# Kernel tuning notes

Measured on AMD Instinct MI355X. Metric: run time of the kernel, lower is better.

## Reference

```python
import jax, jax.numpy as jnp
import numpy as np

N = 100000      # nodes
E = 800000      # directed edges (avg in-degree 8)
FIN = 2         # node features: [type, requests]
C = 32          # embedding_size (per-head out channels)
H = 4           # heads
HC = H * C      # 128
L = 3           # extra conv layers after conv1
D1, D2 = 128, 64
NL = 15         # num_locations
BN_EPS = 1e-5


def _tconv(x, src, dst, ea, qw, qb, kw, kb, vw, vb, ew, skw, skb, bw):
    """PyG TransformerConv with heads=H, concat=True, beta=True, edge_dim."""
    n = x.shape[0]
    q = (x @ qw.T + qb).reshape(n, H, C)
    k = (x @ kw.T + kb).reshape(n, H, C)
    v = (x @ vw.T + vb).reshape(n, H, C)
    e = (ea @ ew.T).reshape(-1, H, C)                     # [E,H,C], lin_edge has no bias
    ke = k[src] + e
    alpha = (q[dst] * ke).sum(-1) / jnp.sqrt(jnp.float32(C))   # [E,H]
    # scatter-softmax over incoming edges of each destination node
    amax = jax.ops.segment_max(alpha, dst, num_segments=n)     # [N,H]
    ex = jnp.exp(alpha - amax[dst])
    denom = jax.ops.segment_sum(ex, dst, num_segments=n)
    attn = ex / jnp.where(denom > 0, denom, 1.0)[dst]
    msg = (v[src] + e) * attn[..., None]                       # [E,H,C]
    out = jax.ops.segment_sum(msg, dst, num_segments=n).reshape(n, HC)
    skip = x @ skw.T + skb                                     # root transform
    beta = jax.nn.sigmoid(jnp.concatenate([out, skip, out - skip], -1) @ bw.T)  # [N,1]
    return beta * skip + (1.0 - beta) * out


def _bn(x, g, b):
    # BatchNorm1d with batch statistics (biased variance), as in torch training math
    mu = x.mean(0)
    var = ((x - mu) ** 2).mean(0)
    return (x - mu) / jnp.sqrt(var + BN_EPS) * g + b


def _forward(node_type, requests, latency, active_mask, edge_index, P):
    (q1_w, q1_b, k1_w, k1_b, v1_w, v1_b, e1_w, skip1_w, skip1_b, beta1_w,
     transf1_w, transf1_b, bn1_g, bn1_b,
     qL_w, qL_b, kL_w, kL_b, vL_w, vL_b, eL_w, skipL_w, skipL_b, betaL_w,
     transfL_w, transfL_b, bnL_g, bnL_b,
     lin1_w, lin1_b, lin2_w, lin2_b, rem_w, rem_b, addp_w, addp_b) = P
    src, dst = edge_index[0], edge_index[1]
    ea = latency[:, None]                                  # [E,1]
    x = jnp.stack([node_type, requests], 1)                # [N,2]
    x = _tconv(x, src, dst, ea, q1_w, q1_b, k1_w, k1_b, v1_w, v1_b,
               e1_w, skip1_w, skip1_b, beta1_w)
    x = _bn(jax.nn.relu(x @ transf1_w.T + transf1_b), bn1_g, bn1_b)
    for i in range(L):
        x = _tconv(x, src, dst, ea, qL_w[i], qL_b[i], kL_w[i], kL_b[i], vL_w[i], vL_b[i],
                   eL_w[i], skipL_w[i], skipL_b[i], betaL_w[i])
        x = _bn(jax.nn.relu(x @ transfL_w[i].T + transfL_b[i]), bnL_g[i], bnL_b[i])
    x = jax.nn.relu(x @ lin1_w.T + lin1_b)                 # dropout(p=0.8) is eval no-op
    x = jax.nn.relu(x @ lin2_w.T + lin2_b)                 # [N,D2]
    mask = active_mask
    head = mask[:NL]
    rm_head = jnp.where(head == 0.0, -jnp.inf, jnp.where(jnp.isneginf(head), 0.0, head))
    remove_mask = mask.at[:NL].set(rm_head)
    removed_logits = (x @ rem_w.T + rem_b)[:, 0] + remove_mask   # [N]
    k1, k2 = jax.random.split(jax.random.key(42))
    action1 = jax.random.categorical(k1, removed_logits)
    mask2 = mask.at[action1].set(0.0)
    proj = jnp.tanh(x[action1] @ addp_w.T + addp_b)              # [D2]
    new_logits = x @ proj + mask2                                # [N]
    action2 = jax.random.categorical(k2, new_logits)
    return removed_logits, new_logits, action1, action2


def setup_inputs() -> dict:
    key = jax.random.key(0)
    ks = iter(jax.random.split(key, 80))
    def nrm(shape, s=0.1):
        return jax.random.normal(next(ks), shape, jnp.float32) * s
    inp = {
        "node_type": jax.random.uniform(next(ks), (N,), jnp.float32),
        "requests": jax.random.uniform(next(ks), (N,), jnp.float32),
        "latency": jax.random.uniform(next(ks), (E,), jnp.float32),
        "active_mask": jnp.zeros((N,), jnp.float32),
        "edge_index": jax.random.randint(next(ks), (2, E), 0, N, dtype=jnp.int32),
        "q1_w": nrm((HC, FIN)), "q1_b": jnp.zeros((HC,)),
        "k1_w": nrm((HC, FIN)), "k1_b": jnp.zeros((HC,)),
        "v1_w": nrm((HC, FIN)), "v1_b": jnp.zeros((HC,)),
        "e1_w": nrm((HC, 1)),
        "skip1_w": nrm((HC, FIN)), "skip1_b": jnp.zeros((HC,)),
        "beta1_w": nrm((1, 3 * HC)),
        "transf1_w": nrm((C, HC)), "transf1_b": jnp.zeros((C,)),
        "bn1_g": jnp.ones((C,)), "bn1_b": jnp.zeros((C,)),
        "qL_w": nrm((L, HC, C)), "qL_b": jnp.zeros((L, HC)),
        "kL_w": nrm((L, HC, C)), "kL_b": jnp.zeros((L, HC)),
        "vL_w": nrm((L, HC, C)), "vL_b": jnp.zeros((L, HC)),
        "eL_w": nrm((L, HC, 1)),
        "skipL_w": nrm((L, HC, C)), "skipL_b": jnp.zeros((L, HC)),
        "betaL_w": nrm((L, 1, 3 * HC)),
        "transfL_w": nrm((L, C, HC)), "transfL_b": jnp.zeros((L, C)),
        "bnL_g": jnp.ones((L, C)), "bnL_b": jnp.zeros((L, C)),
        "lin1_w": nrm((D1, C)), "lin1_b": jnp.zeros((D1,)),
        "lin2_w": nrm((D2, D1)), "lin2_b": jnp.zeros((D2,)),
        "rem_w": nrm((1, D2)), "rem_b": jnp.zeros((1,)),
        "addp_w": nrm((D2, D2)), "addp_b": jnp.zeros((D2,)),
    }
    return inp


def reference(node_type, requests, latency, active_mask, edge_index,
              q1_w, q1_b, k1_w, k1_b, v1_w, v1_b, e1_w, skip1_w, skip1_b, beta1_w,
              transf1_w, transf1_b, bn1_g, bn1_b,
              qL_w, qL_b, kL_w, kL_b, vL_w, vL_b, eL_w, skipL_w, skipL_b, betaL_w,
              transfL_w, transfL_b, bnL_g, bnL_b,
              lin1_w, lin1_b, lin2_w, lin2_b, rem_w, rem_b, addp_w, addp_b):
    P = (q1_w, q1_b, k1_w, k1_b, v1_w, v1_b, e1_w, skip1_w, skip1_b, beta1_w,
         transf1_w, transf1_b, bn1_g, bn1_b,
         qL_w, qL_b, kL_w, kL_b, vL_w, vL_b, eL_w, skipL_w, skipL_b, betaL_w,
         transfL_w, transfL_b, bnL_g, bnL_b,
         lin1_w, lin1_b, lin2_w, lin2_b, rem_w, rem_b, addp_w, addp_b)
    rl, nl, a1, a2 = _forward(node_type, requests, latency, active_mask, edge_index, P)
    log_probs = jnp.stack([jax.nn.log_softmax(rl)[a1], jax.nn.log_softmax(nl)[a2]])
    logits = jnp.stack([rl, nl])      # [2,N]
    actions = jnp.stack([a1, a2])     # [2]
    return logits, actions, log_probs
```

## Files before the change

kernel.cpp:

```cpp
#include <hip/hip_runtime.h>
#include <hip/hip_bf16.h>
#include <math.h>
#include <stdint.h>
#include <limits.h>

#define NN 100000
#define NE 800000
#define PB 512
#define NDB 512
#define NEGBIG (-1e30f)

typedef __hip_bfloat16 bf16;

__device__ __forceinline__ float bf2f(unsigned short u)
{
  union { unsigned v; float f; } x; x.v = ((unsigned)u) << 16; return x.f;
}
__device__ __forceinline__ unsigned short f2bf(float f)
{
  bf16 h = __float2bfloat16(f);
  return *reinterpret_cast<unsigned short*>(&h);
}
__device__ __forceinline__ unsigned pk2(float a, float b)
{
  return (unsigned)f2bf(a) | ((unsigned)f2bf(b) << 16);
}

__device__ __forceinline__ uint2 tf_dev(unsigned k0, unsigned k1, unsigned x0, unsigned x1)
{
  const unsigned ks2 = k0 ^ k1 ^ 0x1BD11BDAu;
#define TFR(r) { x0 += x1; x1 = (x1 << r) | (x1 >> (32 - r)); x1 ^= x0; }
  x0 += k0; x1 += k1;
  TFR(13) TFR(15) TFR(26) TFR(6)
  x0 += k1; x1 += ks2 + 1u;
  TFR(17) TFR(29) TFR(16) TFR(24)
  x0 += ks2; x1 += k0 + 2u;
  TFR(13) TFR(15) TFR(26) TFR(6)
  x0 += k0; x1 += k1 + 3u;
  TFR(17) TFR(29) TFR(16) TFR(24)
  x0 += k1; x1 += ks2 + 4u;
  TFR(13) TFR(15) TFR(26) TFR(6)
  x0 += ks2; x1 += k0 + 5u;
#undef TFR
  return make_uint2(x0, x1);
}

static void tf_host(unsigned k0, unsigned k1, unsigned x0, unsigned x1,
                    unsigned* o0, unsigned* o1)
{
  const unsigned ks2 = k0 ^ k1 ^ 0x1BD11BDAu;
#define TFR(r) { x0 += x1; x1 = (x1 << r) | (x1 >> (32 - r)); x1 ^= x0; }
  x0 += k0; x1 += k1;
  TFR(13) TFR(15) TFR(26) TFR(6)
  x0 += k1; x1 += ks2 + 1u;
  TFR(17) TFR(29) TFR(16) TFR(24)
  x0 += ks2; x1 += k0 + 2u;
  TFR(13) TFR(15) TFR(26) TFR(6)
  x0 += k0; x1 += k1 + 3u;
  TFR(17) TFR(29) TFR(16) TFR(24)
  x0 += k1; x1 += ks2 + 4u;
  TFR(13) TFR(15) TFR(26) TFR(6)
  x0 += ks2; x1 += k0 + 5u;
#undef TFR
  *o0 = x0; *o1 = x1;
}

__device__ __forceinline__ float gumbel_of(unsigned ka, unsigned kb, int i)
{
  uint2 c = tf_dev(ka, kb, 0u, (unsigned)i);
  unsigned bits = c.x ^ c.y;
  float f = __uint_as_float((bits >> 9) | 0x3f800000u) - 1.0f;
  const float TINYF = 1.17549435e-38f;
  float u = fmaxf(TINYF, f + TINYF);
  return -logf(-logf(u));
}

__global__ __launch_bounds__(256) void k_zero2(int* __restrict__ a, int* __restrict__ b)
{
  int i = blockIdx.x * 256 + threadIdx.x;
  if (i < NN) { a[i] = 0; b[i] = 0; }
}

__global__ __launch_bounds__(256) void k_hist(const int* __restrict__ edst, int* __restrict__ deg)
{
  int e = blockIdx.x * 256 + threadIdx.x;
  if (e < NE) atomicAdd(&deg[edst[e]], 1);
}

__global__ __launch_bounds__(1024) void k_scan(const int* __restrict__ deg, int* __restrict__ rowptr)
{
  __shared__ int wsum[16];
  __shared__ int chtot;
  const int t = threadIdx.x;
  const int lane = t & 63;
  const int wv = t >> 6;
  int carry = 0;
  for (int base = 0; base < NN; base += 4096) {
    int i0 = base + t * 4;
    int d0 = 0, d1 = 0, d2 = 0, d3 = 0;
    if (i0 + 3 < NN) { int4 dd = *(const int4*)(deg + i0); d0 = dd.x; d1 = dd.y; d2 = dd.z; d3 = dd.w; }
    else {
      if (i0     < NN) d0 = deg[i0];
      if (i0 + 1 < NN) d1 = deg[i0 + 1];
      if (i0 + 2 < NN) d2 = deg[i0 + 2];
      if (i0 + 3 < NN) d3 = deg[i0 + 3];
    }
    int tsum = d0 + d1 + d2 + d3;
    int sc = tsum;
    #pragma unroll
    for (int off = 1; off < 64; off <<= 1) { int o = __shfl_up(sc, off); if (lane >= off) sc += o; }
    if (lane == 63) wsum[wv] = sc;
    __syncthreads();
    if (wv == 0 && lane < 16) {
      int wval = wsum[lane];
      int wsc = wval;
      #pragma unroll
      for (int off = 1; off < 16; off <<= 1) { int o = __shfl_up(wsc, off); if (lane >= off) wsc += o; }
      if (lane == 15) chtot = wsc;
      wsum[lane] = wsc - wval;
    }
    __syncthreads();
    int excl = carry + wsum[wv] + (sc - tsum);
    if (i0     < NN) rowptr[i0]     = excl;
    if (i0 + 1 < NN) rowptr[i0 + 1] = excl + d0;
    if (i0 + 2 < NN) rowptr[i0 + 2] = excl + d0 + d1;
    if (i0 + 3 < NN) rowptr[i0 + 3] = excl + d0 + d1 + d2;
    carry += chtot;
    __syncthreads();
  }
  if (t == 0) rowptr[NN] = carry;
}

__global__ __launch_bounds__(256) void k_scatter(
    const int* __restrict__ esrc, const int* __restrict__ edst,
    const float* __restrict__ lat, const int* __restrict__ rowptr,
    int* __restrict__ fill, int2* __restrict__ csr)
{
  int e = blockIdx.x * 256 + threadIdx.x;
  if (e >= NE) return;
  int d = edst[e];
  int pos = rowptr[d] + atomicAdd(&fill[d], 1);
  csr[pos] = make_int2(esrc[e], __float_as_int(lat[e]));
}

__global__ __launch_bounds__(256) void k_qkvs_first(
    const float* __restrict__ nt, const float* __restrict__ rq,
    const float* __restrict__ qw, const float* __restrict__ qbv,
    const float* __restrict__ kw, const float* __restrict__ kbv,
    const float* __restrict__ vw, const float* __restrict__ vbv,
    const float* __restrict__ sw, const float* __restrict__ sbv,
    unsigned* __restrict__ q, unsigned short* __restrict__ kv, float* __restrict__ sk)
{
  int idx = blockIdx.x * 256 + threadIdx.x;
  if (idx >= NN * 64) return;
  int n = idx >> 6, l = idx & 63;
  int j0 = 2 * l, j1 = 2 * l + 1;
  float a = nt[n], b = rq[n];
  float q0 = (a * qw[2 * j0] + b * qw[2 * j0 + 1]) + qbv[j0];
  float q1 = (a * qw[2 * j1] + b * qw[2 * j1 + 1]) + qbv[j1];
  q[idx] = pk2(q0, q1);
  ushort4 kvo;
  kvo.x = f2bf((a * kw[2 * j0] + b * kw[2 * j0 + 1]) + kbv[j0]);
  kvo.y = f2bf((a * kw[2 * j1] + b * kw[2 * j1 + 1]) + kbv[j1]);
  kvo.z = f2bf((a * vw[2 * j0] + b * vw[2 * j0 + 1]) + vbv[j0]);
  kvo.w = f2bf((a * vw[2 * j1] + b * vw[2 * j1 + 1]) + vbv[j1]);
  ((ushort4*)kv)[idx] = kvo;
  float2 so;
  so.x = (a * sw[2 * j0] + b * sw[2 * j0 + 1]) + sbv[j0];
  so.y = (a * sw[2 * j1] + b * sw[2 * j1 + 1]) + sbv[j1];
  ((float2*)sk)[idx] = so;
}

#define QP 36
#define WP 33
__global__ __launch_bounds__(256) void k_qkvs3(
    const float* __restrict__ yb, const float* __restrict__ stats,
    const float* __restrict__ bng, const float* __restrict__ bnb,
    const float* __restrict__ wq, const float* __restrict__ bq,
    const float* __restrict__ wk, const float* __restrict__ bk,
    const float* __restrict__ wv, const float* __restrict__ bv,
    const float* __restrict__ wsk, const float* __restrict__ bsk,
    unsigned* __restrict__ oq, unsigned short* __restrict__ okv, float* __restrict__ os)
{
  __shared__ __align__(16) float xs[64 * QP];
  __shared__ __align__(16) float Wl[2 * 128 * WP];

  const int t = threadIdx.x;
  const int nq = t & 15;
  const int chq = t >> 4;
  const int y = blockIdx.y;

  if (y == 1) {
    for (int idx = t; idx < 128 * 32; idx += 256) {
      int c = idx >> 5, k = idx & 31;
      Wl[c * WP + k] = wk[idx];
      Wl[128 * WP + c * WP + k] = wv[idx];
    }
  } else {
    const float* W = (y == 0) ? wq : wsk;
    for (int idx = t; idx < 128 * 32; idx += 256) {
      int c = idx >> 5, k = idx & 31;
      Wl[c * WP + k] = W[idx];
    }
  }

  const int ch0 = (t & 7) * 4;
  float sc[4], sh[4];
  #pragma unroll
  for (int c = 0; c < 4; ++c) {
    int ch = ch0 + c;
    float rsig = 1.0f / stats[32 + ch];
    sc[c] = bng[ch] * rsig;
    sh[c] = bnb[ch] - stats[ch] * sc[c];
  }

  const int ntiles = (NN + 63) / 64;
  for (int tile = blockIdx.x; tile < ntiles; tile += gridDim.x) {
    const int base = tile * 64;
    __syncthreads();
    #pragma unroll
    for (int rep = 0; rep < 2; ++rep) {
      int f = t + rep * 256;
      int n = f >> 3, kq = f & 7;
      int gn = base + n;
      if (gn >= NN) gn = NN - 1;
      float4 v = *(const float4*)(yb + (size_t)gn * 32 + kq * 4);
      v.x = fmaf(v.x, sc[0], sh[0]);
      v.y = fmaf(v.y, sc[1], sh[1]);
      v.z = fmaf(v.z, sc[2], sh[2]);
      v.w = fmaf(v.w, sc[3], sh[3]);
      *(float4*)(xs + n * QP + kq * 4) = v;
    }
    __syncthreads();

    if (y == 1) {
      float ak[4][8], av[4][8];
      #pragma unroll
      for (int s = 0; s < 4; ++s)
        #pragma unroll
        for (int j = 0; j < 8; ++j) { ak[s][j] = bk[chq * 8 + j]; av[s][j] = bv[chq * 8 + j]; }
      #pragma unroll 4
      for (int k2 = 0; k2 < 16; ++k2) {
        const int k = 2 * k2;
        float2 xv[4];
        #pragma unroll
        for (int s = 0; s < 4; ++s) xv[s] = *(const float2*)(xs + (nq + 16 * s) * QP + k);
        #pragma unroll
        for (int j = 0; j < 8; ++j) {
          float2 wk2 = *(const float2*)(Wl + (chq * 8 + j) * WP + k);
          float2 wv2 = *(const float2*)(Wl + 128 * WP + (chq * 8 + j) * WP + k);
          #pragma unroll
          for (int s = 0; s < 4; ++s) {
            ak[s][j] = fmaf(xv[s].x, wk2.x, ak[s][j]);
            ak[s][j] = fmaf(xv[s].y, wk2.y, ak[s][j]);
            av[s][j] = fmaf(xv[s].x, wv2.x, av[s][j]);
            av[s][j] = fmaf(xv[s].y, wv2.y, av[s][j]);
          }
        }
      }
      #pragma unroll
      for (int s = 0; s < 4; ++s) {
        int node = base + nq + 16 * s;
        if (node < NN) {
          uint4 A, B;
          A.x = pk2(ak[s][0], ak[s][1]); A.y = pk2(av[s][0], av[s][1]);
          A.z = pk2(ak[s][2], ak[s][3]); A.w = pk2(av[s][2], av[s][3]);
          B.x = pk2(ak[s][4], ak[s][5]); B.y = pk2(av[s][4], av[s][5]);
          B.z = pk2(ak[s][6], ak[s][7]); B.w = pk2(av[s][6], av[s][7]);
          unsigned short* dst = okv + (size_t)node * 256 + chq * 16;
          *(uint4*)dst = A;
          *(uint4*)(dst + 8) = B;
        }
      }
    } else if (y == 0) {
      float acc[4][8];
      #pragma unroll
      for (int s = 0; s < 4; ++s)
        #pragma unroll
        for (int j = 0; j < 8; ++j) acc[s][j] = bq[chq * 8 + j];
      #pragma unroll 4
      for (int k2 = 0; k2 < 16; ++k2) {
        const int k = 2 * k2;
        float2 xv[4];
        #pragma unroll
        for (int s = 0; s < 4; ++s) xv[s] = *(const float2*)(xs + (nq + 16 * s) * QP + k);
        #pragma unroll
        for (int j = 0; j < 8; ++j) {
          float2 w2 = *(const float2*)(Wl + (chq * 8 + j) * WP + k);
          #pragma unroll
          for (int s = 0; s < 4; ++s) {
            acc[s][j] = fmaf(xv[s].x, w2.x, acc[s][j]);
            acc[s][j] = fmaf(xv[s].y, w2.y, acc[s][j]);
          }
        }
      }
      #pragma unroll
      for (int s = 0; s < 4; ++s) {
        int node = base + nq + 16 * s;
        if (node < NN) {
          uint4 Q;
          Q.x = pk2(acc[s][0], acc[s][1]);
          Q.y = pk2(acc[s][2], acc[s][3]);
          Q.z = pk2(acc[s][4], acc[s][5]);
          Q.w = pk2(acc[s][6], acc[s][7]);
          *(uint4*)(oq + (size_t)node * 64 + chq * 4) = Q;
        }
      }
    } else {
      float acc[4][8];
      #pragma unroll
      for (int s = 0; s < 4; ++s)
        #pragma unroll
        for (int j = 0; j < 8; ++j) acc[s][j] = bsk[chq * 8 + j];
      #pragma unroll 4
      for (int k2 = 0; k2 < 16; ++k2) {
        const int k = 2 * k2;
        float2 xv[4];
        #pragma unroll
        for (int s = 0; s < 4; ++s) xv[s] = *(const float2*)(xs + (nq + 16 * s) * QP + k);
        #pragma unroll
        for (int j = 0; j < 8; ++j) {
          float2 w2 = *(const float2*)(Wl + (chq * 8 + j) * WP + k);
          #pragma unroll
          for (int s = 0; s < 4; ++s) {
            acc[s][j] = fmaf(xv[s].x, w2.x, acc[s][j]);
            acc[s][j] = fmaf(xv[s].y, w2.y, acc[s][j]);
          }
        }
      }
      #pragma unroll
      for (int s = 0; s < 4; ++s) {
        int node = base + nq + 16 * s;
        if (node < NN) {
          float* dst = os + (size_t)node * 128 + chq * 8;
          *(float4*)dst = make_float4(acc[s][0], acc[s][1], acc[s][2], acc[s][3]);
          *(float4*)(dst + 4) = make_float4(acc[s][4], acc[s][5], acc[s][6], acc[s][7]);
        }
      }
    }
  }
}

__global__ __launch_bounds__(256) void k_lin1d(
    const float* __restrict__ yb, const float* __restrict__ stats,
    const float* __restrict__ bng, const float* __restrict__ bnb,
    const float* __restrict__ W, const float* __restrict__ B, float* __restrict__ O)
{
  __shared__ __align__(16) float xs[64 * QP];
  __shared__ __align__(16) float Wl[128 * WP];
  const int t = threadIdx.x;
  const int nq = t & 15;
  const int chq = t >> 4;
  for (int idx = t; idx < 128 * 32; idx += 256) {
    int c = idx >> 5, k = idx & 31;
    Wl[c * WP + k] = W[idx];
  }
  const int ch0 = (t & 7) * 4;
  float sc[4], sh[4];
  #pragma unroll
  for (int c = 0; c < 4; ++c) {
    int ch = ch0 + c;
    float rsig = 1.0f / stats[32 + ch];
    sc[c] = bng[ch] * rsig;
    sh[c] = bnb[ch] - stats[ch] * sc[c];
  }
  const int ntiles = (NN + 63) / 64;
  for (int tile = blockIdx.x; tile < ntiles; tile += gridDim.x) {
    const int base = tile * 64;
    __syncthreads();
    #pragma unroll
    for (int rep = 0; rep < 2; ++rep) {
      int f = t + rep * 256;
      int n = f >> 3, kq = f & 7;
      int gn = base + n;
      if (gn >= NN) gn = NN - 1;
      float4 v = *(const float4*)(yb + (size_t)gn * 32 + kq * 4);
      v.x = fmaf(v.x, sc[0], sh[0]);
      v.y = fmaf(v.y, sc[1], sh[1]);
      v.z = fmaf(v.z, sc[2], sh[2]);
      v.w = fmaf(v.w, sc[3], sh[3]);
      *(float4*)(xs + n * QP + kq * 4) = v;
    }
    __syncthreads();
    float acc[4][8];
    #pragma unroll
    for (int s = 0; s < 4; ++s)
      #pragma unroll
      for (int j = 0; j < 8; ++j) acc[s][j] = B[chq * 8 + j];
    #pragma unroll 4
    for (int k2 = 0; k2 < 16; ++k2) {
      const int k = 2 * k2;
      float2 xv[4];
      #pragma unroll
      for (int s = 0; s < 4; ++s) xv[s] = *(const float2*)(xs + (nq + 16 * s) * QP + k);
      #pragma unroll
      for (int j = 0; j < 8; ++j) {
        float2 w2 = *(const float2*)(Wl + (chq * 8 + j) * WP + k);
        #pragma unroll
        for (int s = 0; s < 4; ++s) {
          acc[s][j] = fmaf(xv[s].x, w2.x, acc[s][j]);
          acc[s][j] = fmaf(xv[s].y, w2.y, acc[s][j]);
        }
      }
    }
    #pragma unroll
    for (int s = 0; s < 4; ++s) {
      int node = base + nq + 16 * s;
      if (node < NN) {
        float* dst = O + (size_t)node * 128 + chq * 8;
        *(float4*)dst = make_float4(fmaxf(acc[s][0], 0.f), fmaxf(acc[s][1], 0.f),
                                    fmaxf(acc[s][2], 0.f), fmaxf(acc[s][3], 0.f));
        *(float4*)(dst + 4) = make_float4(fmaxf(acc[s][4], 0.f), fmaxf(acc[s][5], 0.f),
                                          fmaxf(acc[s][6], 0.f), fmaxf(acc[s][7], 0.f));
      }
    }
  }
}

#define XPITCH 132
#define WPITCH 130
template<int COUT, bool STATS, bool REM>
__global__ __launch_bounds__(256) void k_dense(
    const float* __restrict__ xin, const float* __restrict__ W,
    const float* __restrict__ bias, float* __restrict__ out,
    double* __restrict__ psum, double* __restrict__ psq,
    const float* __restrict__ rw, const float* __restrict__ rb,
    const float* __restrict__ amask, float* __restrict__ rl)
{
  constexpr int JB = COUT / 16;
  __shared__ __align__(16) float xs[64 * XPITCH];
  __shared__ float Ws[COUT * WPITCH];
  __shared__ float rem_lds[REM ? 16 * 64 : 1];

  const int t = threadIdx.x;
  const int nq = t & 15;
  const int chq = t >> 4;

  for (int idx = t; idx < COUT * 128; idx += 256) {
    int c = idx >> 7, k = idx & 127;
    Ws[c * WPITCH + k] = W[idx];
  }
  float bj[JB];
  float rwj[REM ? JB : 1];
  #pragma unroll
  for (int j = 0; j < JB; ++j) {
    bj[j] = bias[chq * JB + j];
    if (REM) rwj[j] = rw[chq * JB + j];
  }
  double sd[STATS ? JB : 1], sq[STATS ? JB : 1];
  if (STATS) {
    #pragma unroll
    for (int j = 0; j < JB; ++j) { sd[j] = 0.0; sq[j] = 0.0; }
  }

  const int ntiles = (NN + 63) / 64;
  for (int tile = blockIdx.x; tile < ntiles; tile += gridDim.x) {
    const int base = tile * 64;
    __syncthreads();
    #pragma unroll
    for (int r = 0; r < 8; ++r) {
      int f = t + r * 256;
      int n = f >> 5, kq = f & 31;
      int gn = base + n;
      if (gn >= NN) gn = NN - 1;
      float4 v = *(const float4*)(xin + (size_t)gn * 128 + kq * 4);
      *(float4*)(xs + n * XPITCH + kq * 4) = v;
    }
    __syncthreads();

    float acc[4][JB];
    #pragma unroll
    for (int s = 0; s < 4; ++s)
      #pragma unroll
      for (int j = 0; j < JB; ++j) acc[s][j] = bj[j];

    #pragma unroll 8
    for (int k2 = 0; k2 < 64; ++k2) {
      const int k = 2 * k2;
      float2 xv[4];
      #pragma unroll
      for (int s = 0; s < 4; ++s)
        xv[s] = *(const float2*)(xs + (nq + 16 * s) * XPITCH + k);
      float2 wv[JB];
      #pragma unroll
      for (int j = 0; j < JB; ++j)
        wv[j] = *(const float2*)(Ws + (chq * JB + j) * WPITCH + k);
      #pragma unroll
      for (int s = 0; s < 4; ++s)
        #pragma unroll
        for (int j = 0; j < JB; ++j) {
          acc[s][j] = fmaf(xv[s].x, wv[j].x, acc[s][j]);
          acc[s][j] = fmaf(xv[s].y, wv[j].y, acc[s][j]);
        }
    }

    #pragma unroll
    for (int s = 0; s < 4; ++s) {
      const int node = base + nq + 16 * s;
      const bool ok = node < NN;
      #pragma unroll
      for (int j = 0; j < JB; ++j) acc[s][j] = fmaxf(acc[s][j], 0.f);
      if (ok) {
        if (COUT == 32) {
          *(float2*)(out + (size_t)node * 32 + chq * 2) = make_float2(acc[s][0], acc[s][1]);
        } else {
          *(float4*)(out + (size_t)node * 64 + chq * 4) =
              make_float4(acc[s][0], acc[s][1], acc[s][2], acc[s][3]);
        }
      }
      if (STATS && ok) {
        #pragma unroll
        for (int j = 0; j < JB; ++j) {
          sd[j] += (double)acc[s][j];
          sq[j] += (double)acc[s][j] * (double)acc[s][j];
        }
      }
      if (REM) {
        float p = 0.f;
        #pragma unroll
        for (int j = 0; j < JB; ++j) p = fmaf(acc[s][j], rwj[j], p);
        rem_lds[chq * 64 + nq + 16 * s] = p;
      }
    }

    if (REM) {
      __syncthreads();
      if (t < 64) {
        int node = base + t;
        if (node < NN) {
          float v = rb[0];
          #pragma unroll
          for (int c = 0; c < 16; ++c) v += rem_lds[c * 64 + t];
          float mv = amask[node];
          float mterm;
          if (node < 15) mterm = (mv == 0.f) ? -INFINITY : ((mv == -INFINITY) ? 0.f : mv);
          else mterm = mv;
          rl[node] = fmaxf(v + mterm, NEGBIG);
        }
      }
    }
  }

  if (STATS) {
    __shared__ double sred[256 * 2];
    __syncthreads();
    #pragma unroll
    for (int j = 0; j < JB; ++j) { sred[t * 2 + j] = sd[j]; }
    __syncthreads();
    if (t < 32) {
      int cq = t >> 1, j = t & 1;
      double a = 0.0;
      #pragma unroll
      for (int n = 0; n < 16; ++n) a += sred[(cq * 16 + n) * 2 + j];
      psum[blockIdx.x * 32 + t] = a;
    }
    __syncthreads();
    #pragma unroll
    for (int j = 0; j < JB; ++j) { sred[t * 2 + j] = sq[j]; }
    __syncthreads();
    if (t < 32) {
      int cq = t >> 1, j = t & 1;
      double a = 0.0;
      #pragma unroll
      for (int n = 0; n < 16; ++n) a += sred[(cq * 16 + n) * 2 + j];
      psq[blockIdx.x * 32 + t] = a;
    }
  }
}

__global__ __launch_bounds__(1024) void k_stats2(
    const double* __restrict__ psum, const double* __restrict__ psq, float* __restrict__ stats)
{
  const int t = threadIdx.x;
  const int ch = t & 31;
  const int chunk = t >> 5;
  double s = 0.0, q = 0.0;
  for (int b = chunk; b < NDB; b += 32) { s += psum[b * 32 + ch]; q += psq[b * 32 + ch]; }
  __shared__ double rs[1024];
  __shared__ double rq[1024];
  rs[t] = s; rq[t] = q;
  __syncthreads();
  for (int off = 16; off > 0; off >>= 1) {
    if (chunk < off) { rs[t] += rs[t + off * 32]; rq[t] += rq[t + off * 32]; }
    __syncthreads();
  }
  if (t < 32) {
    double mu = rs[t] / (double)NN;
    double var = rq[t] / (double)NN - mu * mu;
    if (var < 0.0) var = 0.0;
    stats[t] = (float)mu;
    stats[32 + t] = sqrtf((float)var + 1e-5f);
  }
}

__global__ __launch_bounds__(256) void k_attn(
    const unsigned* __restrict__ qb, const unsigned short* __restrict__ kvb,
    float* __restrict__ skh,
    const int* __restrict__ rowptr, const int2* __restrict__ csr,
    const float* __restrict__ ew, const float* __restrict__ bw)
{
  const int wid = (blockIdx.x * 256 + threadIdx.x) >> 6;
  const int lane = threadIdx.x & 63;
  if (wid >= NN) return;
  const unsigned qu = qb[(size_t)wid * 64 + lane];
  const float qx = bf2f((unsigned short)(qu & 0xffffu));
  const float qy = bf2f((unsigned short)(qu >> 16));
  const float2 ew2 = ((const float2*)ew)[lane];
  const ushort4* kvp = (const ushort4*)kvb;
  const int p0 = rowptr[wid], p1 = rowptr[wid + 1];

  float s = 0.f, accx = 0.f, accy = 0.f;
  const float iscale = 0.17677669529663689f;

#define EDGE_BODY(cc, kv) {                                            \
    float lat = __int_as_float(cc.y);                                  \
    float e0 = lat * ew2.x, e1 = lat * ew2.y;                          \
    float kx = bf2f(kv.x) + e0, ky = bf2f(kv.y) + e1;                  \
    float part = qx * kx + qy * ky;                                    \
    part += __shfl_xor(part, 1);                                       \
    part += __shfl_xor(part, 2);                                       \
    part += __shfl_xor(part, 4);                                       \
    part += __shfl_xor(part, 8);                                       \
    float pt = __expf(part * iscale);                                  \
    float vx = bf2f(kv.z) + e0, vy = bf2f(kv.w) + e1;                  \
    s += pt;                                                           \
    accx = fmaf(pt, vx, accx);                                         \
    accy = fmaf(pt, vy, accy); }

  int p = p0;
  for (; p + 7 < p1; p += 8) {
    int2 c0 = csr[p],     c1 = csr[p + 1], c2 = csr[p + 2], c3 = csr[p + 3];
    int2 c4 = csr[p + 4], c5 = csr[p + 5], c6 = csr[p + 6], c7 = csr[p + 7];
    ushort4 kv0 = kvp[(size_t)c0.x * 64 + lane];
    ushort4 kv1 = kvp[(size_t)c1.x * 64 + lane];
    ushort4 kv2 = kvp[(size_t)c2.x * 64 + lane];
    ushort4 kv3 = kvp[(size_t)c3.x * 64 + lane];
    ushort4 kv4 = kvp[(size_t)c4.x * 64 + lane];
    ushort4 kv5 = kvp[(size_t)c5.x * 64 + lane];
    ushort4 kv6 = kvp[(size_t)c6.x * 64 + lane];
    ushort4 kv7 = kvp[(size_t)c7.x * 64 + lane];
    EDGE_BODY(c0, kv0)
    EDGE_BODY(c1, kv1)
    EDGE_BODY(c2, kv2)
    EDGE_BODY(c3, kv3)
    EDGE_BODY(c4, kv4)
    EDGE_BODY(c5, kv5)
    EDGE_BODY(c6, kv6)
    EDGE_BODY(c7, kv7)
  }
  for (; p + 3 < p1; p += 4) {
    int2 c0 = csr[p], c1 = csr[p + 1], c2 = csr[p + 2], c3 = csr[p + 3];
    ushort4 kv0 = kvp[(size_t)c0.x * 64 + lane];
    ushort4 kv1 = kvp[(size_t)c1.x * 64 + lane];
    ushort4 kv2 = kvp[(size_t)c2.x * 64 + lane];
    ushort4 kv3 = kvp[(size_t)c3.x * 64 + lane];
    EDGE_BODY(c0, kv0)
    EDGE_BODY(c1, kv1)
    EDGE_BODY(c2, kv2)
    EDGE_BODY(c3, kv3)
  }
  for (; p < p1; ++p) {
    int2 c0 = csr[p];
    ushort4 kv0 = kvp[(size_t)c0.x * 64 + lane];
    EDGE_BODY(c0, kv0)
  }
#undef EDGE_BODY

  float inv = (s > 0.f) ? (1.0f / s) : 1.0f;
  float ox = accx * inv, oy = accy * inv;

  float2* sk2p = (float2*)skh;
  float2 skv = sk2p[(size_t)wid * 64 + lane];
  const float2* bw2 = (const float2*)bw;
  float2 b1 = bw2[lane], b2 = bw2[64 + lane], b3 = bw2[128 + lane];
  float part = b1.x * ox + b1.y * oy + b2.x * skv.x + b2.y * skv.y
             + b3.x * (ox - skv.x) + b3.y * (oy - skv.y);
  #pragma unroll
  for (int off = 1; off < 64; off <<= 1) part += __shfl_xor(part, off);
  float beta = 1.f / (1.f + __expf(-part));
  float2 hv;
  hv.x = beta * skv.x + (1.f - beta) * ox;
  hv.y = beta * skv.y + (1.f - beta) * oy;
  sk2p[(size_t)wid * 64 + lane] = hv;
}

__global__ __launch_bounds__(256) void k_pass(
    const float* __restrict__ lg,
    float* __restrict__ pm, float* __restrict__ ps, float* __restrict__ pg, int* __restrict__ pidx,
    unsigned ka, unsigned kb)
{
  float m = -INFINITY, s = 0.f, g = -INFINITY; int gi = INT_MAX; bool hg = false;
  for (int i = blockIdx.x * 256 + threadIdx.x; i < NN; i += gridDim.x * 256) {
    float v = lg[i];
    if (v > m) { s = (m == -INFINITY) ? 1.f : fmaf(s, expf(m - v), 1.f); m = v; }
    else if (v != -INFINITY) s += expf(v - m);
    float tot = v + gumbel_of(ka, kb, i);
    if (!hg || tot > g || (tot == g && i < gi)) { g = tot; gi = i; hg = true; }
  }
  __shared__ float sm[256], ss[256], sg[256]; __shared__ int si[256];
  int t = threadIdx.x;
  sm[t] = m; ss[t] = s; sg[t] = g; si[t] = gi;
  __syncthreads();
  for (int off = 128; off > 0; off >>= 1) {
    if (t < off) {
      float m2 = sm[t + off], s2 = ss[t + off];
      float M = fmaxf(sm[t], m2);
      float sn = 0.f;
      if (M != -INFINITY) {
        if (sm[t] != -INFINITY) sn += ss[t] * expf(sm[t] - M);
        if (m2 != -INFINITY) sn += s2 * expf(m2 - M);
      }
      sm[t] = M; ss[t] = sn;
      float g2 = sg[t + off]; int i2 = si[t + off];
      if (g2 > sg[t] || (g2 == sg[t] && i2 < si[t])) { sg[t] = g2; si[t] = i2; }
    }
    __syncthreads();
  }
  if (t == 0) { pm[blockIdx.x] = sm[0]; ps[blockIdx.x] = ss[0]; pg[blockIdx.x] = sg[0]; pidx[blockIdx.x] = si[0]; }
}

__global__ __launch_bounds__(PB) void k_choose(
    const float* __restrict__ lg,
    const float* __restrict__ pm, const float* __restrict__ ps,
    const float* __restrict__ pg, const int* __restrict__ pidx,
    float* __restrict__ act_out, float* __restrict__ lp_out, int* __restrict__ a_scr)
{
  __shared__ float sm[PB], ss[PB], sg[PB]; __shared__ int si[PB];
  int t = threadIdx.x;
  sm[t] = pm[t]; ss[t] = ps[t]; sg[t] = pg[t]; si[t] = pidx[t];
  __syncthreads();
  for (int off = PB / 2; off > 0; off >>= 1) {
    if (t < off) {
      float m2 = sm[t + off], s2 = ss[t + off];
      float M = fmaxf(sm[t], m2);
      float sn = 0.f;
      if (M != -INFINITY) {
        if (sm[t] != -INFINITY) sn += ss[t] * expf(sm[t] - M);
        if (m2 != -INFINITY) sn += s2 * expf(m2 - M);
      }
      sm[t] = M; ss[t] = sn;
      float g2 = sg[t + off]; int i2 = si[t + off];
      if (g2 > sg[t] || (g2 == sg[t] && i2 < si[t])) { sg[t] = g2; si[t] = i2; }
    }
    __syncthreads();
  }
  if (t == 0) {
    int a = si[0];
    a_scr[0] = a;
    act_out[0] = (float)a;
    lp_out[0] = (lg[a] - sm[0]) - logf(ss[0]);
  }
}

__global__ void k_proj(const float* __restrict__ xf, const int* __restrict__ a1p,
                       const float* __restrict__ aw, const float* __restrict__ ab,
                       float* __restrict__ proj)
{
  __shared__ float xs[64];
  int t = threadIdx.x;
  int a1 = a1p[0];
  xs[t] = xf[(size_t)a1 * 64 + t];
  __syncthreads();
  float acc = 0.f;
  #pragma unroll
  for (int i = 0; i < 64; ++i) acc = fmaf(xs[i], aw[t * 64 + i], acc);
  proj[t] = tanhf(acc + ab[t]);
}

__global__ __launch_bounds__(256) void k_nl(
    const float* __restrict__ xf, const float* __restrict__ proj,
    const float* __restrict__ amask, const int* __restrict__ a1p, float* __restrict__ nl)
{
  int wid = (blockIdx.x * 256 + threadIdx.x) >> 6;
  int lane = threadIdx.x & 63;
  if (wid >= NN) return;
  float part = xf[(size_t)wid * 64 + lane] * proj[lane];
  #pragma unroll
  for (int off = 1; off < 64; off <<= 1) part += __shfl_xor(part, off);
  if (lane == 0) {
    int a1 = a1p[0];
    float mv = (wid == a1) ? 0.f : amask[wid];
    nl[wid] = fmaxf(part + mv, NEGBIG);
  }
}

extern "C" void kernel_launch(void* const* d_in, const int* in_sizes, int n_in,
                              void* d_out, int out_size, void* d_ws, size_t ws_size,
                              hipStream_t stream)
{
  (void)in_sizes; (void)n_in; (void)out_size; (void)ws_size;

  const float* node_type = (const float*)d_in[0];
  const float* requests  = (const float*)d_in[1];
  const float* latency   = (const float*)d_in[2];
  const float* amask     = (const float*)d_in[3];
  const int*   eidx      = (const int*)d_in[4];
  const int* esrc = eidx;
  const int* edst = eidx + NE;

  const float* q1_w = (const float*)d_in[5];  const float* q1_b = (const float*)d_in[6];
  const float* k1_w = (const float*)d_in[7];  const float* k1_b = (const float*)d_in[8];
  const float* v1_w = (const float*)d_in[9];  const float* v1_b = (const float*)d_in[10];
  const float* e1_w = (const float*)d_in[11];
  const float* sk1_w = (const float*)d_in[12]; const float* sk1_b = (const float*)d_in[13];
  const float* be1_w = (const float*)d_in[14];
  const float* tf1_w = (const float*)d_in[15]; const float* tf1_b = (const float*)d_in[16];
  const float* bn1_g = (const float*)d_in[17]; const float* bn1_b = (const float*)d_in[18];
  const float* qL_w = (const float*)d_in[19]; const float* qL_b = (const float*)d_in[20];
  const float* kL_w = (const float*)d_in[21]; const float* kL_b = (const float*)d_in[22];
  const float* vL_w = (const float*)d_in[23]; const float* vL_b = (const float*)d_in[24];
  const float* eL_w = (const float*)d_in[25];
  const float* skL_w = (const float*)d_in[26]; const float* skL_b = (const float*)d_in[27];
  const float* beL_w = (const float*)d_in[28];
  const float* tfL_w = (const float*)d_in[29]; const float* tfL_b = (const float*)d_in[30];
  const float* bnL_g = (const float*)d_in[31]; const float* bnL_b = (const float*)d_in[32];
  const float* l1_w = (const float*)d_in[33]; const float* l1_b = (const float*)d_in[34];
  const float* l2_w = (const float*)d_in[35]; const float* l2_b = (const float*)d_in[36];
  const float* rem_w = (const float*)d_in[37]; const float* rem_b = (const float*)d_in[38];
  const float* ap_w = (const float*)d_in[39]; const float* ap_b = (const float*)d_in[40];

  char* ws = (char*)d_ws;
  size_t off = 0;
  auto alloc = [&](size_t bytes) -> void* {
    void* p = ws + off;
    off += (bytes + 255) & ~(size_t)255;
    return p;
  };
  unsigned* qbuf = (unsigned*)alloc((size_t)NN * 64 * 4);
  unsigned short* kvbuf = (unsigned short*)alloc((size_t)NN * 256 * 2);
  float* skb  = (float*)alloc((size_t)NN * 128 * 4);
  float* yb   = (float*)alloc((size_t)NN * 32 * 4);
  int*   rowptr = (int*)alloc((size_t)(NN + 1) * 4);
  int*   deg    = (int*)alloc((size_t)NN * 4);
  int*   fill   = (int*)alloc((size_t)NN * 4);
  int2*  csr    = (int2*)alloc((size_t)NE * 8);
  double* psum = (double*)alloc((size_t)NDB * 32 * 8);
  double* psq  = (double*)alloc((size_t)NDB * 32 * 8);
  float* stats = (float*)alloc(64 * 4);
  float* pm = (float*)alloc(PB * 4);
  float* ps = (float*)alloc(PB * 4);
  float* pg = (float*)alloc(PB * 4);
  int*   pidx = (int*)alloc(PB * 4);
  float* proj = (float*)alloc(64 * 4);
  int*   a_scr = (int*)alloc(2 * 4);
  float* y1 = skb;
  float* xf = (float*)kvbuf;

  unsigned k1a, k1b, k2a, k2b;
  tf_host(0u, 42u, 0u, 0u, &k1a, &k1b);
  tf_host(0u, 42u, 0u, 1u, &k2a, &k2b);

  float* dout = (float*)d_out;

  k_zero2<<<(NN + 255) / 256, 256, 0, stream>>>(deg, fill);
  k_hist<<<(NE + 255) / 256, 256, 0, stream>>>(edst, deg);
  k_scan<<<1, 1024, 0, stream>>>(deg, rowptr);
  k_scatter<<<(NE + 255) / 256, 256, 0, stream>>>(esrc, edst, latency, rowptr, fill, csr);

  k_qkvs_first<<<(NN * 64 + 255) / 256, 256, 0, stream>>>(
      node_type, requests, q1_w, q1_b, k1_w, k1_b, v1_w, v1_b, sk1_w, sk1_b,
      qbuf, kvbuf, skb);
  k_attn<<<NN / 4, 256, 0, stream>>>(qbuf, kvbuf, skb, rowptr, csr, e1_w, be1_w);
  k_dense<32, true, false><<<NDB, 256, 0, stream>>>(skb, tf1_w, tf1_b, yb, psum, psq,
                                                    nullptr, nullptr, nullptr, nullptr);
  k_stats2<<<1, 1024, 0, stream>>>(psum, psq, stats);

  for (int i = 0; i < 3; ++i) {
    const float* g = (i == 0) ? bn1_g : bnL_g + (i - 1) * 32;
    const float* b = (i == 0) ? bn1_b : bnL_b + (i - 1) * 32;
    k_qkvs3<<<dim3(NDB, 3), 256, 0, stream>>>(
        yb, stats, g, b,
        qL_w + i * 4096, qL_b + i * 128,
        kL_w + i * 4096, kL_b + i * 128,
        vL_w + i * 4096, vL_b + i * 128,
        skL_w + i * 4096, skL_b + i * 128,
        qbuf, kvbuf, skb);
    k_attn<<<NN / 4, 256, 0, stream>>>(qbuf, kvbuf, skb, rowptr, csr,
                                       eL_w + i * 128, beL_w + i * 384);
    k_dense<32, true, false><<<NDB, 256, 0, stream>>>(skb, tfL_w + i * 4096, tfL_b + i * 32,
                                                      yb, psum, psq,
                                                      nullptr, nullptr, nullptr, nullptr);
    k_stats2<<<1, 1024, 0, stream>>>(psum, psq, stats);
  }

  k_lin1d<<<NDB, 256, 0, stream>>>(yb, stats, bnL_g + 2 * 32, bnL_b + 2 * 32, l1_w, l1_b, y1);
  k_dense<64, false, true><<<NDB, 256, 0, stream>>>(y1, l2_w, l2_b, xf, nullptr, nullptr,
                                                    rem_w, rem_b, amask, dout);

  k_pass<<<PB, 256, 0, stream>>>(dout, pm, ps, pg, pidx, k1a, k1b);
  k_choose<<<1, PB, 0, stream>>>(dout, pm, ps, pg, pidx,
                                 dout + 2 * NN, dout + 2 * NN + 2, a_scr);
  k_proj<<<1, 64, 0, stream>>>(xf, a_scr, ap_w, ap_b, proj);
  k_nl<<<NN / 4, 256, 0, stream>>>(xf, proj, amask, a_scr, dout + NN);
  k_pass<<<PB, 256, 0, stream>>>(dout + NN, pm, ps, pg, pidx, k2a, k2b);
  k_choose<<<1, PB, 0, stream>>>(dout + NN, pm, ps, pg, pidx,
                                 dout + 2 * NN + 1, dout + 2 * NN + 3, a_scr + 1);
}
```

Baseline: 872.8 us.

## Fuse transformer-output linear and BN partial stats into attention kernel

The attention kernel now runs the 128->32 transf linear, ReLU and per-block BatchNorm partial sums directly on each block's four node outputs kept in shared memory. This removes the separate k_dense pass, along with the write and re-read of the 128-wide h buffer for every layer. The projection step is also folded into k_choose to drop one launch. In exchange, each attention block reloads the 32x128 weight into LDS, and k_stats2 must now reduce 25000 partial rows instead of 512, so that single-block kernel does more serial work.

Result: slower. 2.019 ms (+131.3%).

```diff
diff --git a/kernel.cpp b/kernel.cpp
--- a/kernel.cpp
+++ b/kernel.cpp
@@ -8,6 +8,7 @@
 #define NE 800000
 #define PB 512
 #define NDB 512
+#define NAB (NN / 4)
 #define NEGBIG (-1e30f)
 
 typedef __hip_bfloat16 bf16;
@@ -419,11 +420,10 @@
 
 #define XPITCH 132
 #define WPITCH 130
-template<int COUT, bool STATS, bool REM>
+template<int COUT, bool REM>
 __global__ __launch_bounds__(256) void k_dense(
     const float* __restrict__ xin, const float* __restrict__ W,
     const float* __restrict__ bias, float* __restrict__ out,
-    double* __restrict__ psum, double* __restrict__ psq,
     const float* __restrict__ rw, const float* __restrict__ rb,
     const float* __restrict__ amask, float* __restrict__ rl)
 {
@@ -446,11 +446,6 @@
   for (int j = 0; j < JB; ++j) {
     bj[j] = bias[chq * JB + j];
     if (REM) rwj[j] = rw[chq * JB + j];
-  }
-  double sd[STATS ? JB : 1], sq[STATS ? JB : 1];
-  if (STATS) {
-    #pragma unroll
-    for (int j = 0; j < JB; ++j) { sd[j] = 0.0; sq[j] = 0.0; }
   }
 
   const int ntiles = (NN + 63) / 64;
@@ -506,13 +501,6 @@
         } else {
           *(float4*)(out + (size_t)node * 64 + chq * 4) =
               make_float4(acc[s][0], acc[s][1], acc[s][2], acc[s][3]);
-        }
-      }
-      if (STATS && ok) {
-        #pragma unroll
-        for (int j = 0; j < JB; ++j) {
-          sd[j] += (double)acc[s][j];
-          sq[j] += (double)acc[s][j] * (double)acc[s][j];
         }
       }
       if (REM) {
@@ -540,32 +528,6 @@
       }
     }
   }
-
-  if (STATS) {
-    __shared__ double sred[256 * 2];
-    __syncthreads();
-    #pragma unroll
-    for (int j = 0; j < JB; ++j) { sred[t * 2 + j] = sd[j]; }
-    __syncthreads();
-    if (t < 32) {
-      int cq = t >> 1, j = t & 1;
-      double a = 0.0;
-      #pragma unroll
-      for (int n = 0; n < 16; ++n) a += sred[(cq * 16 + n) * 2 + j];
-      psum[blockIdx.x * 32 + t] = a;
-    }
-    __syncthreads();
-    #pragma unroll
-    for (int j = 0; j < JB; ++j) { sred[t * 2 + j] = sq[j]; }
-    __syncthreads();
-    if (t < 32) {
-      int cq = t >> 1, j = t & 1;
-      double a = 0.0;
-      #pragma unroll
-      for (int n = 0; n < 16; ++n) a += sred[(cq * 16 + n) * 2 + j];
-      psq[blockIdx.x * 32 + t] = a;
-    }
-  }
 }
 
 __global__ __launch_bounds__(1024) void k_stats2(
@@ -575,7 +537,7 @@
   const int ch = t & 31;
   const int chunk = t >> 5;
   double s = 0.0, q = 0.0;
-  for (int b = chunk; b < NDB; b += 32) { s += psum[b * 32 + ch]; q += psq[b * 32 + ch]; }
+  for (int b = chunk; b < NAB; b += 32) { s += psum[b * 32 + ch]; q += psq[b * 32 + ch]; }
   __shared__ double rs[1024];
   __shared__ double rq[1024];
   rs[t] = s; rq[t] = q;
@@ -593,15 +555,31 @@
   }
 }
 
-__global__ __launch_bounds__(256) void k_attn(
+#define HP 132
+#define TWP 130
+__global__ __launch_bounds__(256) void k_attn_tf(
     const unsigned* __restrict__ qb, const unsigned short* __restrict__ kvb,
-    float* __restrict__ skh,
+    const float* __restrict__ skb,
     const int* __restrict__ rowptr, const int2* __restrict__ csr,
-    const float* __restrict__ ew, const float* __restrict__ bw)
-{
-  const int wid = (blockIdx.x * 256 + threadIdx.x) >> 6;
-  const int lane = threadIdx.x & 63;
-  if (wid >= NN) return;
+    const float* __restrict__ ew, const float* __restrict__ bw,
+    const float* __restrict__ tw, const float* __restrict__ tb,
+    float* __restrict__ yb, double* __restrict__ psum, double* __restrict__ psq)
+{
+  __shared__ __align__(16) float hs[4 * HP];
+  __shared__ __align__(16) float Ws[32 * TWP];
+  __shared__ double rs[128];
+  __shared__ double rq[128];
+
+  const int t = threadIdx.x;
+  const int w = t >> 6;
+  const int lane = t & 63;
+  const int wid = blockIdx.x * 4 + w;
+
+  for (int idx = t; idx < 32 * 128; idx += 256) {
+    int c = idx >> 7, k = idx & 127;
+    Ws[c * TWP + k] = tw[idx];
+  }
+
   const unsigned qu = qb[(size_t)wid * 64 + lane];
   const float qx = bf2f((unsigned short)(qu & 0xffffu));
   const float qy = bf2f((unsigned short)(qu >> 16));
@@ -669,8 +647,7 @@
   float inv = (s > 0.f) ? (1.0f / s) : 1.0f;
   float ox = accx * inv, oy = accy * inv;
 
-  float2* sk2p = (float2*)skh;
-  float2 skv = sk2p[(size_t)wid * 64 + lane];
+  float2 skv = ((const float2*)skb)[(size_t)wid * 64 + lane];
   const float2* bw2 = (const float2*)bw;
   float2 b1 = bw2[lane], b2 = bw2[64 + lane], b3 = bw2[128 + lane];
   float part = b1.x * ox + b1.y * oy + b2.x * skv.x + b2.y * skv.y
@@ -681,7 +658,31 @@
   float2 hv;
   hv.x = beta * skv.x + (1.f - beta) * ox;
   hv.y = beta * skv.y + (1.f - beta) * oy;
-  sk2p[(size_t)wid * 64 + lane] = hv;
+  *(float2*)(hs + w * HP + 2 * lane) = hv;
+  __syncthreads();
+
+  {
+    const int n = w;
+    const int ch = lane >> 1;
+    const int half = lane & 1;
+    const float* hrow = hs + n * HP + half * 64;
+    const float* wrow = Ws + ch * TWP + half * 64;
+    float acc = 0.f;
+    #pragma unroll 16
+    for (int k = 0; k < 64; ++k) acc = fmaf(hrow[k], wrow[k], acc);
+    acc += __shfl_xor(acc, 1);
+    if (half == 0) {
+      float r = fmaxf(acc + tb[ch], 0.f);
+      yb[(size_t)wid * 32 + ch] = r;
+      rs[ch * 4 + n] = (double)r;
+      rq[ch * 4 + n] = (double)r * (double)r;
+    }
+  }
+  __syncthreads();
+  if (t < 32) {
+    psum[(size_t)blockIdx.x * 32 + t] = rs[t * 4] + rs[t * 4 + 1] + rs[t * 4 + 2] + rs[t * 4 + 3];
+    psq [(size_t)blockIdx.x * 32 + t] = rq[t * 4] + rq[t * 4 + 1] + rq[t * 4 + 2] + rq[t * 4 + 3];
+  }
 }
 
 __global__ __launch_bounds__(256) void k_pass(
@@ -723,9 +724,12 @@
     const float* __restrict__ lg,
     const float* __restrict__ pm, const float* __restrict__ ps,
     const float* __restrict__ pg, const int* __restrict__ pidx,
-    float* __restrict__ act_out, float* __restrict__ lp_out, int* __restrict__ a_scr)
+    float* __restrict__ act_out, float* __restrict__ lp_out, int* __restrict__ a_scr,
+    const float* __restrict__ xf, const float* __restrict__ aw,
+    const float* __restrict__ ab, float* __restrict__ proj)
 {
   __shared__ float sm[PB], ss[PB], sg[PB]; __shared__ int si[PB];
+  __shared__ float xs2[64];
   int t = threadIdx.x;
   sm[t] = pm[t]; ss[t] = ps[t]; sg[t] = pg[t]; si[t] = pidx[t];
   __syncthreads();
@@ -750,21 +754,18 @@
     act_out[0] = (float)a;
     lp_out[0] = (lg[a] - sm[0]) - logf(ss[0]);
   }
-}
-
-__global__ void k_proj(const float* __restrict__ xf, const int* __restrict__ a1p,
-                       const float* __restrict__ aw, const float* __restrict__ ab,
-                       float* __restrict__ proj)
-{
-  __shared__ float xs[64];
-  int t = threadIdx.x;
-  int a1 = a1p[0];
-  xs[t] = xf[(size_t)a1 * 64 + t];
-  __syncthreads();
-  float acc = 0.f;
-  #pragma unroll
-  for (int i = 0; i < 64; ++i) acc = fmaf(xs[i], aw[t * 64 + i], acc);
-  proj[t] = tanhf(acc + ab[t]);
+  if (aw != nullptr) {
+    __syncthreads();
+    int a = si[0];
+    if (t < 64) xs2[t] = xf[(size_t)a * 64 + t];
+    __syncthreads();
+    if (t < 64) {
+      float acc = 0.f;
+      #pragma unroll
+      for (int i = 0; i < 64; ++i) acc = fmaf(xs2[i], aw[t * 64 + i], acc);
+      proj[t] = tanhf(acc + ab[t]);
+    }
+  }
 }
 
 __global__ __launch_bounds__(256) void k_nl(
@@ -834,8 +835,8 @@
   int*   deg    = (int*)alloc((size_t)NN * 4);
   int*   fill   = (int*)alloc((size_t)NN * 4);
   int2*  csr    = (int2*)alloc((size_t)NE * 8);
-  double* psum = (double*)alloc((size_t)NDB * 32 * 8);
-  double* psq  = (double*)alloc((size_t)NDB * 32 * 8);
+  double* psum = (double*)alloc((size_t)NAB * 32 * 8);
+  double* psq  = (double*)alloc((size_t)NAB * 32 * 8);
   float* stats = (float*)alloc(64 * 4);
   float* pm = (float*)alloc(PB * 4);
   float* ps = (float*)alloc(PB * 4);
@@ -860,9 +861,8 @@
   k_qkvs_first<<<(NN * 64 + 255) / 256, 256, 0, stream>>>(
       node_type, requests, q1_w, q1_b, k1_w, k1_b, v1_w, v1_b, sk1_w, sk1_b,
       qbuf, kvbuf, skb);
-  k_attn<<<NN / 4, 256, 0, stream>>>(qbuf, kvbuf, skb, rowptr, csr, e1_w, be1_w);
-  k_dense<32, true, false><<<NDB, 256, 0, stream>>>(skb, tf1_w, tf1_b, yb, psum, psq,
-                                                    nullptr, nullptr, nullptr, nullptr);
+  k_attn_tf<<<NAB, 256, 0, stream>>>(qbuf, kvbuf, skb, rowptr, csr, e1_w, be1_w,
+                                     tf1_w, tf1_b, yb, psum, psq);
   k_stats2<<<1, 1024, 0, stream>>>(psum, psq, stats);
 
   for (int i = 0; i < 3; ++i) {
@@ -875,24 +875,23 @@
         vL_w + i * 4096, vL_b + i * 128,
         skL_w + i * 4096, skL_b + i * 128,
         qbuf, kvbuf, skb);
-    k_attn<<<NN / 4, 256, 0, stream>>>(qbuf, kvbuf, skb, rowptr, csr,
-                                       eL_w + i * 128, beL_w + i * 384);
-    k_dense<32, true, false><<<NDB, 256, 0, stream>>>(skb, tfL_w + i * 4096, tfL_b + i * 32,
-                                                      yb, psum, psq,
-                                                      nullptr, nullptr, nullptr, nullptr);
+    k_attn_tf<<<NAB, 256, 0, stream>>>(qbuf, kvbuf, skb, rowptr, csr,
+                                       eL_w + i * 128, beL_w + i * 384,
+                                       tfL_w + i * 4096, tfL_b + i * 32, yb, psum, psq);
     k_stats2<<<1, 1024, 0, stream>>>(psum, psq, stats);
   }
 
   k_lin1d<<<NDB, 256, 0, stream>>>(yb, stats, bnL_g + 2 * 32, bnL_b + 2 * 32, l1_w, l1_b, y1);
-  k_dense<64, false, true><<<NDB, 256, 0, stream>>>(y1, l2_w, l2_b, xf, nullptr, nullptr,
-                                                    rem_w, rem_b, amask, dout);
+  k_dense<64, true><<<NDB, 256, 0, stream>>>(y1, l2_w, l2_b, xf,
+                                             rem_w, rem_b, amask, dout);
 
   k_pass<<<PB, 256, 0, stream>>>(dout, pm, ps, pg, pidx, k1a, k1b);
   k_choose<<<1, PB, 0, stream>>>(dout, pm, ps, pg, pidx,
-                                 dout + 2 * NN, dout + 2 * NN + 2, a_scr);
-  k_proj<<<1, 64, 0, stream>>>(xf, a_scr, ap_w, ap_b, proj);
+                                 dout + 2 * NN, dout + 2 * NN + 2, a_scr,
+                                 xf, ap_w, ap_b, proj);
   k_nl<<<NN / 4, 256, 0, stream>>>(xf, proj, amask, a_scr, dout + NN);
   k_pass<<<PB, 256, 0, stream>>>(dout + NN, pm, ps, pg, pidx, k2a, k2b);
   k_choose<<<1, PB, 0, stream>>>(dout + NN, pm, ps, pg, pidx,
-                                 dout + 2 * NN + 1, dout + 2 * NN + 3, a_scr + 1);
-}
+                                 dout + 2 * NN + 1, dout + 2 * NN + 3, a_scr + 1,
+                                 nullptr, nullptr, nullptr, nullptr);
+}
```
